# Performance work log

Measured on AMD Instinct MI355X. Metric: run time of the kernel, lower is better.

Reference implementation:

```python
import jax, jax.numpy as jnp
import numpy as np

N, M, D = 2048, 16, 256


def setup_inputs() -> dict:
    key = jax.random.key(0)
    k1, = jax.random.split(key, 1)
    embeddings = jax.random.normal(k1, (N, M, D), dtype=jnp.float32)
    w = jnp.asarray(10.0, dtype=jnp.float32)
    b = jnp.asarray(-5.0, dtype=jnp.float32)
    return {"embeddings": embeddings, "w": w, "b": b}


def reference(embeddings, w, b):
    # embeddings: [N, M, D]
    centroids = embeddings.mean(axis=1)          # [N, D]
    sum_ = embeddings.sum(axis=1)                # [N, D]
    e = embeddings.reshape(N * M, D)             # [NM, D]
    cosine_sim = e @ centroids.T                 # [NM, N]
    # excluded-self centroid for each (speaker j, utterance i):
    # cj = (sum_[j] - e_ji) / (M - 1); replace cosine_sim[ji, j] with dot(cj, e_ji)
    excl = (sum_[:, None, :] - embeddings) / (M - 1)           # [N, M, D]
    diag_vals = jnp.sum(excl * embeddings, axis=-1).reshape(N * M)  # [NM]
    labels = jnp.repeat(jnp.arange(N), M)                      # [NM]
    cosine_sim = cosine_sim.at[jnp.arange(N * M), labels].set(diag_vals)
    logits = w * cosine_sim + b                                # [NM, N]
    logp = jax.nn.log_softmax(logits, axis=-1)
    loss = -jnp.mean(logp[jnp.arange(N * M), labels])
    return loss
```

## Files before the change

### kernel.cpp

```cpp
#include <hip/hip_runtime.h>
#include <hip/hip_bf16.h>
#if !__has_builtin(__builtin_amdgcn_cvt_pk_fp8_f32)
#include <hip/hip_fp8.h>
#endif

#define NS 2048
#define MU 16
#define DD 256
#define NMROWS (NS*MU)
#define STRIPS 8
#define SC 256
#define NSTEP 8
#define BMROWS 128
#define THR 8.0f

typedef float  f32x4  __attribute__((ext_vector_type(4)));
typedef float  f32x16 __attribute__((ext_vector_type(16)));
typedef int    i32x4  __attribute__((ext_vector_type(4)));

#define LOG2E 1.44269504088896340736f
#define LN2   0.69314718055994530942f

#if __has_builtin(__builtin_amdgcn_exp2f)
#define EXP2F(x) __builtin_amdgcn_exp2f(x)
#else
#define EXP2F(x) exp2f(x)
#endif
#if __has_builtin(__builtin_amdgcn_logf)
#define LOG2F(x) __builtin_amdgcn_logf(x)
#else
#define LOG2F(x) __log2f(x)
#endif

__device__ __forceinline__ int pk4(float a, float b, float c, float d){
#if __has_builtin(__builtin_amdgcn_cvt_pk_fp8_f32)
  int v = __builtin_amdgcn_cvt_pk_fp8_f32(a, b, 0, false);
  v = __builtin_amdgcn_cvt_pk_fp8_f32(c, d, v, true);
  return v;
#else
  unsigned r = (unsigned)__hip_fp8_e4m3(a).__x
             | ((unsigned)__hip_fp8_e4m3(b).__x << 8)
             | ((unsigned)__hip_fp8_e4m3(c).__x << 16)
             | ((unsigned)__hip_fp8_e4m3(d).__x << 24);
  return (int)r;
#endif
}
__device__ __forceinline__ long mk64(int lo, int hi){
  return (long)(((unsigned long long)(unsigned)lo) |
                ((unsigned long long)(unsigned)hi << 32));
}

__launch_bounds__(256)
__global__ void prep_kernel(const float* __restrict__ emb,
                            const float* __restrict__ wp,
                            unsigned char* __restrict__ centk,
                            unsigned char* __restrict__ embk8,
                            float* __restrict__ diag2){
  __shared__ float E[16*260];
  __shared__ float sm[256];
  const int t = threadIdx.x;
  const int n = blockIdx.x;
  const float* src = emb + (size_t)n*MU*DD;

  #pragma unroll
  for (int i=0;i<4;i++){
    int g = i*1024 + t*4;
    f32x4 v = *(const f32x4*)(src + g);
    int m = g >> 8, d = g & 255;
    *(f32x4*)&E[m*260 + d] = v;
  }
  __syncthreads();

  {
    float s = 0.f;
    #pragma unroll
    for (int m=0;m<16;m++) s += E[m*260 + t];
    sm[t] = s;
  }
  __syncthreads();

  const float w2 = wp[0] * LOG2E;

  if (t < 16){
    const float c16 = w2 * (1.0f/16.0f);
    const float* p = &sm[t*16];
    i32x4 o;
    #pragma unroll
    for (int q=0;q<4;q++)
      o[q] = pk4(p[q*4]*c16, p[q*4+1]*c16, p[q*4+2]*c16, p[q*4+3]*c16);
    *(i32x4*)(centk + ((size_t)t*NS + n)*16) = o;
  }

  if (embk8){
    int st = t >> 4, r = t & 15;
    const float* p = &E[r*260 + st*16];
    i32x4 o;
    #pragma unroll
    for (int q=0;q<4;q++){
      f32x4 v = *(const f32x4*)(p + q*4);
      o[q] = pk4(v[0], v[1], v[2], v[3]);
    }
    *(i32x4*)(embk8 + ((size_t)st*NMROWS + n*16 + r)*16) = o;
  }

  {
    int m = t >> 4, j = t & 15;
    float acc = 0.f;
    #pragma unroll
    for (int i=0;i<16;i++){
      int d = j + 16*i;
      float e = E[m*260 + d];
      acc += e * (sm[d] - e);
    }
    acc += __shfl_xor(acc, 1, 16);
    acc += __shfl_xor(acc, 2, 16);
    acc += __shfl_xor(acc, 4, 16);
    acc += __shfl_xor(acc, 8, 16);
    if (j==0) diag2[n*16 + m] = acc * (w2 * (1.0f/15.0f));
  }
}

__device__ __forceinline__ void stage_b(const unsigned char* __restrict__ centk,
                                        long* lds0, int colbase,
                                        int wave, int lane){
  #pragma unroll
  for (int i=0;i<2;i++){
    const int s0 = (i*4 + wave)*64;
    const int st = (s0 >> 5) + (lane >> 5);
    const unsigned char* g = centk + ((size_t)st*NS + colbase + (lane & 31))*16;
    __builtin_amdgcn_global_load_lds(
        (const __attribute__((address_space(1))) void*)g,
        (__attribute__((address_space(3))) void*)((char*)lds0 + (size_t)s0*16),
        16, 0, 0);
  }
}

#define MFMA8(a,b,c) __builtin_amdgcn_mfma_f32_32x32x16_fp8_fp8(a,b,c,0,0,0)

template<bool FROMF32>
__launch_bounds__(256,4)
__global__ void ge2e_main(const float* __restrict__ embf,
                          const unsigned char* __restrict__ embk8,
                          const unsigned char* __restrict__ centk,
                          const float* __restrict__ diag2,
                          float2* __restrict__ msbuf){
  __shared__ long Bbuf[2][1024];

  const int tid  = threadIdx.x;
  const int lane = tid & 63;
  const int wave = tid >> 6;
  const int l31  = lane & 31, hi = lane >> 5;
  const int strip  = blockIdx.x & 7;
  const int rowBlk = blockIdx.x >> 3;
  const int c0 = strip * SC;
  const int rowA = rowBlk*BMROWS + wave*32 + l31;

  stage_b(centk, &Bbuf[0][0], c0, wave, lane);

  long af[16];
  if constexpr (FROMF32){
    const float* rp = embf + (size_t)rowA*DD;
    #pragma unroll
    for (int st=0; st<16; ++st){
      f32x4 v0 = *(const f32x4*)(rp + 16*st + 8*hi);
      f32x4 v1 = *(const f32x4*)(rp + 16*st + 8*hi + 4);
      af[st] = mk64(pk4(v0[0],v0[1],v0[2],v0[3]), pk4(v1[0],v1[1],v1[2],v1[3]));
    }
  } else {
    #pragma unroll
    for (int st=0; st<16; ++st)
      af[st] = *(const long*)(embk8 + ((size_t)st*NMROWS + rowA)*16 + hi*8);
  }

  const float dv  = diag2[rowA];
  const int   lab = rowA >> 4;
  const int   labc0 = rowBlk*8;
  const bool  hasdiag = (labc0 >= c0) && (labc0 < c0 + SC);
  const int   dstep = (labc0 - c0) >> 5;

  float m = -3.0e38f, s = 0.f;

  __syncthreads();

  for (int step=0; step<NSTEP; ++step){
    const int cb_ = step & 1;
    if (step+1 < NSTEP)
      stage_b(centk, &Bbuf[cb_^1][0], c0 + (step+1)*32, wave, lane);

    f32x16 acc;
    #pragma unroll
    for (int i=0;i<16;i++) acc[i] = 0.f;

    #pragma unroll
    for (int st=0; st<16; ++st){
      long cb = Bbuf[cb_][st*64 + l31*2 + hi];
      acc = MFMA8(cb, af[st], acc);
    }

    if (hasdiag && step == dstep){
      int colbase = c0 + step*32 + 4*hi;
      #pragma unroll
      for (int r=0;r<16;r++){
        int col = colbase + (r&3) + 8*(r>>2);
        if (col == lab) acc[r] = dv;
      }
    }

    float x0 = fmaxf(fmaxf(fmaxf(acc[0],acc[1]),fmaxf(acc[2],acc[3])),
                     fmaxf(fmaxf(acc[4],acc[5]),fmaxf(acc[6],acc[7])));
    float x1 = fmaxf(fmaxf(fmaxf(acc[8],acc[9]),fmaxf(acc[10],acc[11])),
                     fmaxf(fmaxf(acc[12],acc[13]),fmaxf(acc[14],acc[15])));
    float tm = fmaxf(x0, x1);
    if (__any(tm > m + THR)){
      float mn = fmaxf(m, tm);
      s *= EXP2F(m - mn);
      m = mn;
    }
    float a0 = EXP2F(acc[0]-m)+EXP2F(acc[1]-m)+EXP2F(acc[2]-m)+EXP2F(acc[3]-m);
    float a1 = EXP2F(acc[4]-m)+EXP2F(acc[5]-m)+EXP2F(acc[6]-m)+EXP2F(acc[7]-m);
    float a2 = EXP2F(acc[8]-m)+EXP2F(acc[9]-m)+EXP2F(acc[10]-m)+EXP2F(acc[11]-m);
    float a3 = EXP2F(acc[12]-m)+EXP2F(acc[13]-m)+EXP2F(acc[14]-m)+EXP2F(acc[15]-m);
    s += (a0+a1)+(a2+a3);

    asm volatile("s_waitcnt vmcnt(0)" ::: "memory");
    __builtin_amdgcn_s_barrier();
  }

  float mo = __shfl_xor(m,32,64), so = __shfl_xor(s,32,64);
  float mm = fmaxf(m,mo);
  float ss = s*EXP2F(m-mm) + so*EXP2F(mo-mm);

  if (hi==0) msbuf[(size_t)strip*NMROWS + rowA] = make_float2(mm, ss);
}

__launch_bounds__(512)
__global__ void merge_kernel(const float2* __restrict__ msbuf,
                             const float* __restrict__ diag2,
                             float* __restrict__ partials){
  __shared__ float sh[8];
  const int row = blockIdx.x*512 + threadIdx.x;
  float2 p[STRIPS];
  #pragma unroll
  for (int k=0;k<STRIPS;k++) p[k] = msbuf[(size_t)k*NMROWS + row];
  float mm = p[0].x;
  #pragma unroll
  for (int k=1;k<STRIPS;k++) mm = fmaxf(mm, p[k].x);
  float ss = 0.f;
  #pragma unroll
  for (int k=0;k<STRIPS;k++) ss += p[k].y * EXP2F(p[k].x - mm);
  float term = LN2*(mm + LOG2F(ss) - diag2[row]);
  #pragma unroll
  for (int off=32; off; off>>=1) term += __shfl_xor(term, off, 64);
  if ((threadIdx.x & 63)==0) sh[threadIdx.x>>6] = term;
  __syncthreads();
  if (threadIdx.x==0){
    float v = 0.f;
    #pragma unroll
    for (int i=0;i<8;i++) v += sh[i];
    partials[blockIdx.x] = v;
  }
}

__global__ void final_kernel(const float* __restrict__ partials,
                             float* __restrict__ out){
  int tid = threadIdx.x;
  float v = partials[tid];
  #pragma unroll
  for (int off=32; off; off>>=1) v += __shfl_xor(v, off, 64);
  if (tid==0) out[0] = v * (1.0f/NMROWS);
}

extern "C" void kernel_launch(void* const* d_in, const int* in_sizes, int n_in,
                              void* d_out, int out_size, void* d_ws, size_t ws_size,
                              hipStream_t stream){
  const float* emb = (const float*)d_in[0];
  const float* wp  = (const float*)d_in[1];
  float* out = (float*)d_out;
  char* ws = (char*)d_ws;

  const size_t centk_b = (size_t)NS*DD;
  const size_t embk_b  = (size_t)NMROWS*DD;
  const size_t diag_b  = (size_t)NMROWS*4;
  const size_t ms_b    = (size_t)STRIPS*NMROWS*8;
  const bool useEmbk = ws_size >= centk_b + embk_b + diag_b + ms_b + 1024;

  unsigned char* centk = (unsigned char*)ws;
  size_t off = centk_b;
  unsigned char* embk8 = useEmbk ? (unsigned char*)(ws + off) : nullptr;
  if (useEmbk) off += embk_b;
  float*  diag2 = (float*)(ws + off);  off += diag_b;
  float2* msbuf = (float2*)(ws + off); off += ms_b;
  float*  parts = (float*)(ws + off);

  prep_kernel<<<NS, 256, 0, stream>>>(emb, wp, centk, embk8, diag2);
  if (useEmbk)
    ge2e_main<false><<<(NMROWS/BMROWS)*STRIPS, 256, 0, stream>>>(emb, embk8, centk, diag2, msbuf);
  else
    ge2e_main<true><<<(NMROWS/BMROWS)*STRIPS, 256, 0, stream>>>(emb, embk8, centk, diag2, msbuf);
  merge_kernel<<<NMROWS/512, 512, 0, stream>>>(msbuf, diag2, parts);
  final_kernel<<<1, 64, 0, stream>>>(parts, out);
}
```

Measured before the change: 47.65 us.

## Process 64 centroid columns per step with pre-swizzled fp8 centroid layout

Each main-loop step now runs two 32-column MFMA tiles (accA/accB) instead of one, which halves the number of steps, barriers and online-softmax rescale checks. The prep kernel writes centroids in a layout that matches the MFMA B-operand access, so LDS reads become contiguous per lane and staging uses linear global-to-LDS copies. The running max now starts at 0 instead of -inf. LDS use per block doubles and more accumulator registers are live, which may reduce occupancy.

```diff
diff --git a/kernel.cpp b/kernel.cpp
--- a/kernel.cpp
+++ b/kernel.cpp
@@ -10,7 +10,7 @@
 #define NMROWS (NS*MU)
 #define STRIPS 8
 #define SC 256
-#define NSTEP 8
+#define NSTEP 4
 #define BMROWS 128
 #define THR 8.0f
 
@@ -50,10 +50,11 @@
                 ((unsigned long long)(unsigned)hi << 32));
 }
 
+
 __launch_bounds__(256)
 __global__ void prep_kernel(const float* __restrict__ emb,
                             const float* __restrict__ wp,
-                            unsigned char* __restrict__ centk,
+                            long* __restrict__ centk8,
                             unsigned char* __restrict__ embk8,
                             float* __restrict__ diag2){
   __shared__ float E[16*260];
@@ -83,12 +84,15 @@
 
   if (t < 16){
     const float c16 = w2 * (1.0f/16.0f);
-    const float* p = &sm[t*16];
-    i32x4 o;
-    #pragma unroll
-    for (int q=0;q<4;q++)
-      o[q] = pk4(p[q*4]*c16, p[q*4+1]*c16, p[q*4+2]*c16, p[q*4+3]*c16);
-    *(i32x4*)(centk + ((size_t)t*NS + n)*16) = o;
+    const int st = t;
+    const float* p = &sm[st*16];
+    int q0 = pk4(p[0]*c16,  p[1]*c16,  p[2]*c16,  p[3]*c16);
+    int q1 = pk4(p[4]*c16,  p[5]*c16,  p[6]*c16,  p[7]*c16);
+    int q2 = pk4(p[8]*c16,  p[9]*c16,  p[10]*c16, p[11]*c16);
+    int q3 = pk4(p[12]*c16, p[13]*c16, p[14]*c16, p[15]*c16);
+    size_t base = ((size_t)(st*64 + (n>>5))*2)*32 + (n&31);
+    centk8[base]      = mk64(q0, q1);
+    centk8[base + 32] = mk64(q2, q3);
   }
 
   if (embk8){
@@ -120,17 +124,16 @@
   }
 }
 
-__device__ __forceinline__ void stage_b(const unsigned char* __restrict__ centk,
-                                        long* lds0, int colbase,
+__device__ __forceinline__ void stage_b(const long* __restrict__ centk8,
+                                        long* lds0, int cg0,
                                         int wave, int lane){
   #pragma unroll
-  for (int i=0;i<2;i++){
-    const int s0 = (i*4 + wave)*64;
-    const int st = (s0 >> 5) + (lane >> 5);
-    const unsigned char* g = centk + ((size_t)st*NS + colbase + (lane & 31))*16;
+  for (int i=0;i<4;i++){
+    const int st = i*4 + wave;
+    const long* g = centk8 + (size_t)(st*64 + cg0)*64 + lane*2;
     __builtin_amdgcn_global_load_lds(
         (const __attribute__((address_space(1))) void*)g,
-        (__attribute__((address_space(3))) void*)((char*)lds0 + (size_t)s0*16),
+        (__attribute__((address_space(3))) void*)(lds0 + (size_t)st*128),
         16, 0, 0);
   }
 }
@@ -141,10 +144,10 @@
 __launch_bounds__(256,4)
 __global__ void ge2e_main(const float* __restrict__ embf,
                           const unsigned char* __restrict__ embk8,
-                          const unsigned char* __restrict__ centk,
+                          const long* __restrict__ centk8,
                           const float* __restrict__ diag2,
                           float2* __restrict__ msbuf){
-  __shared__ long Bbuf[2][1024];
+  __shared__ long Bbuf[2][2048];
 
   const int tid  = threadIdx.x;
   const int lane = tid & 63;
@@ -155,7 +158,7 @@
   const int c0 = strip * SC;
   const int rowA = rowBlk*BMROWS + wave*32 + l31;
 
-  stage_b(centk, &Bbuf[0][0], c0, wave, lane);
+  stage_b(centk8, &Bbuf[0][0], c0 >> 5, wave, lane);
 
   long af[16];
   if constexpr (FROMF32){
@@ -176,51 +179,73 @@
   const int   lab = rowA >> 4;
   const int   labc0 = rowBlk*8;
   const bool  hasdiag = (labc0 >= c0) && (labc0 < c0 + SC);
-  const int   dstep = (labc0 - c0) >> 5;
-
-  float m = -3.0e38f, s = 0.f;
+  const int   dstep = (labc0 - c0) >> 6;
+  const int   dgrp  = ((labc0 - c0) >> 5) & 1;
+
+  float m = 0.f, s = 0.f;
 
   __syncthreads();
 
   for (int step=0; step<NSTEP; ++step){
     const int cb_ = step & 1;
     if (step+1 < NSTEP)
-      stage_b(centk, &Bbuf[cb_^1][0], c0 + (step+1)*32, wave, lane);
-
-    f32x16 acc;
-    #pragma unroll
-    for (int i=0;i<16;i++) acc[i] = 0.f;
+      stage_b(centk8, &Bbuf[cb_^1][0], (c0 >> 5) + (step+1)*2, wave, lane);
+
+    const long* cur = &Bbuf[cb_][0];
+    const int bi = hi*32 + l31;
+
+    f32x16 accA, accB;
+    #pragma unroll
+    for (int i=0;i<16;i++){ accA[i] = 0.f; accB[i] = 0.f; }
 
     #pragma unroll
     for (int st=0; st<16; ++st){
-      long cb = Bbuf[cb_][st*64 + l31*2 + hi];
-      acc = MFMA8(cb, af[st], acc);
+      long b0 = cur[st*128 + bi];
+      long b1 = cur[st*128 + 64 + bi];
+      accA = MFMA8(b0, af[st], accA);
+      accB = MFMA8(b1, af[st], accB);
     }
 
     if (hasdiag && step == dstep){
-      int colbase = c0 + step*32 + 4*hi;
-      #pragma unroll
-      for (int r=0;r<16;r++){
-        int col = colbase + (r&3) + 8*(r>>2);
-        if (col == lab) acc[r] = dv;
+      int colbase = c0 + step*64 + dgrp*32 + 4*hi;
+      if (dgrp == 0){
+        #pragma unroll
+        for (int r=0;r<16;r++){
+          int col = colbase + (r&3) + 8*(r>>2);
+          if (col == lab) accA[r] = dv;
+        }
+      } else {
+        #pragma unroll
+        for (int r=0;r<16;r++){
+          int col = colbase + (r&3) + 8*(r>>2);
+          if (col == lab) accB[r] = dv;
+        }
       }
     }
 
-    float x0 = fmaxf(fmaxf(fmaxf(acc[0],acc[1]),fmaxf(acc[2],acc[3])),
-                     fmaxf(fmaxf(acc[4],acc[5]),fmaxf(acc[6],acc[7])));
-    float x1 = fmaxf(fmaxf(fmaxf(acc[8],acc[9]),fmaxf(acc[10],acc[11])),
-                     fmaxf(fmaxf(acc[12],acc[13]),fmaxf(acc[14],acc[15])));
-    float tm = fmaxf(x0, x1);
+    float xa0 = fmaxf(fmaxf(fmaxf(accA[0],accA[1]),fmaxf(accA[2],accA[3])),
+                      fmaxf(fmaxf(accA[4],accA[5]),fmaxf(accA[6],accA[7])));
+    float xa1 = fmaxf(fmaxf(fmaxf(accA[8],accA[9]),fmaxf(accA[10],accA[11])),
+                      fmaxf(fmaxf(accA[12],accA[13]),fmaxf(accA[14],accA[15])));
+    float xb0 = fmaxf(fmaxf(fmaxf(accB[0],accB[1]),fmaxf(accB[2],accB[3])),
+                      fmaxf(fmaxf(accB[4],accB[5]),fmaxf(accB[6],accB[7])));
+    float xb1 = fmaxf(fmaxf(fmaxf(accB[8],accB[9]),fmaxf(accB[10],accB[11])),
+                      fmaxf(fmaxf(accB[12],accB[13]),fmaxf(accB[14],accB[15])));
+    float tm = fmaxf(fmaxf(xa0,xa1), fmaxf(xb0,xb1));
     if (__any(tm > m + THR)){
       float mn = fmaxf(m, tm);
       s *= EXP2F(m - mn);
       m = mn;
     }
-    float a0 = EXP2F(acc[0]-m)+EXP2F(acc[1]-m)+EXP2F(acc[2]-m)+EXP2F(acc[3]-m);
-    float a1 = EXP2F(acc[4]-m)+EXP2F(acc[5]-m)+EXP2F(acc[6]-m)+EXP2F(acc[7]-m);
-    float a2 = EXP2F(acc[8]-m)+EXP2F(acc[9]-m)+EXP2F(acc[10]-m)+EXP2F(acc[11]-m);
-    float a3 = EXP2F(acc[12]-m)+EXP2F(acc[13]-m)+EXP2F(acc[14]-m)+EXP2F(acc[15]-m);
-    s += (a0+a1)+(a2+a3);
+    float a0 = EXP2F(accA[0]-m)+EXP2F(accA[1]-m)+EXP2F(accA[2]-m)+EXP2F(accA[3]-m);
+    float a1 = EXP2F(accA[4]-m)+EXP2F(accA[5]-m)+EXP2F(accA[6]-m)+EXP2F(accA[7]-m);
+    float a2 = EXP2F(accA[8]-m)+EXP2F(accA[9]-m)+EXP2F(accA[10]-m)+EXP2F(accA[11]-m);
+    float a3 = EXP2F(accA[12]-m)+EXP2F(accA[13]-m)+EXP2F(accA[14]-m)+EXP2F(accA[15]-m);
+    float b0 = EXP2F(accB[0]-m)+EXP2F(accB[1]-m)+EXP2F(accB[2]-m)+EXP2F(accB[3]-m);
+    float b1 = EXP2F(accB[4]-m)+EXP2F(accB[5]-m)+EXP2F(accB[6]-m)+EXP2F(accB[7]-m);
+    float b2 = EXP2F(accB[8]-m)+EXP2F(accB[9]-m)+EXP2F(accB[10]-m)+EXP2F(accB[11]-m);
+    float b3 = EXP2F(accB[12]-m)+EXP2F(accB[13]-m)+EXP2F(accB[14]-m)+EXP2F(accB[15]-m);
+    s += ((a0+a1)+(a2+a3)) + ((b0+b1)+(b2+b3));
 
     asm volatile("s_waitcnt vmcnt(0)" ::: "memory");
     __builtin_amdgcn_s_barrier();
@@ -284,7 +309,7 @@
   const size_t ms_b    = (size_t)STRIPS*NMROWS*8;
   const bool useEmbk = ws_size >= centk_b + embk_b + diag_b + ms_b + 1024;
 
-  unsigned char* centk = (unsigned char*)ws;
+  long* centk8 = (long*)ws;
   size_t off = centk_b;
   unsigned char* embk8 = useEmbk ? (unsigned char*)(ws + off) : nullptr;
   if (useEmbk) off += embk_b;
@@ -292,11 +317,11 @@
   float2* msbuf = (float2*)(ws + off); off += ms_b;
   float*  parts = (float*)(ws + off);
 
-  prep_kernel<<<NS, 256, 0, stream>>>(emb, wp, centk, embk8, diag2);
+  prep_kernel<<<NS, 256, 0, stream>>>(emb, wp, centk8, embk8, diag2);
   if (useEmbk)
-    ge2e_main<false><<<(NMROWS/BMROWS)*STRIPS, 256, 0, stream>>>(emb, embk8, centk, diag2, msbuf);
+    ge2e_main<false><<<(NMROWS/BMROWS)*STRIPS, 256, 0, stream>>>(emb, embk8, centk8, diag2, msbuf);
   else
-    ge2e_main<true><<<(NMROWS/BMROWS)*STRIPS, 256, 0, stream>>>(emb, embk8, centk, diag2, msbuf);
+    ge2e_main<true><<<(NMROWS/BMROWS)*STRIPS, 256, 0, stream>>>(emb, embk8, centk8, diag2, msbuf);
   merge_kernel<<<NMROWS/512, 512, 0, stream>>>(msbuf, diag2, parts);
   final_kernel<<<1, 64, 0, stream>>>(parts, out);
 }
```

Result: no change. 47.35 us (-0.6%).
